# Optimization experiments

Measured on AMD Instinct MI355X. Metric: run time of the kernel, lower is better.

Reference implementation:

```python
import jax, jax.numpy as jnp
import numpy as np

N_NODES = 100000


def gcn_conv(x, src, dst, W, b, n):
    # PyG GCNConv: add self-loops, symmetric deg^-1/2 normalization,
    # linear transform, scatter-add aggregation, bias.
    loops = jnp.arange(n, dtype=src.dtype)
    s = jnp.concatenate([src, loops])
    d = jnp.concatenate([dst, loops])
    deg = jax.ops.segment_sum(jnp.ones_like(s, dtype=x.dtype), d, num_segments=n)
    dinv = jnp.where(deg > 0, jax.lax.rsqrt(deg), 0.0)
    norm = dinv[s] * dinv[d]  # [E+N]
    h = x @ W  # [N, out]
    msgs = h[s] * norm[:, None]  # gather + scale, [E+N, out]
    out = jax.ops.segment_sum(msgs, d, num_segments=n)  # scatter-add
    return out + b


def setup_inputs() -> dict:
    key = jax.random.key(0)
    k1, k2, k3, k4 = jax.random.split(key, 4)
    n, e = N_NODES, 1600000
    cin, chid, cout = 256, 128, 64
    x = jax.random.normal(k1, (n, cin), dtype=jnp.float32)
    edge_index = jax.random.randint(k2, (2, e), 0, n, dtype=jnp.int64)
    W1 = jax.random.normal(k3, (cin, chid), dtype=jnp.float32) * (1.0 / np.sqrt(cin))
    b1 = jnp.zeros((chid,), dtype=jnp.float32)
    W2 = jax.random.normal(k4, (chid, cout), dtype=jnp.float32) * (1.0 / np.sqrt(chid))
    b2 = jnp.zeros((cout,), dtype=jnp.float32)
    return {"x": x, "edge_index": edge_index, "W1": W1, "b1": b1, "W2": W2, "b2": b2}


def reference(x, edge_index, W1, b1, W2, b2):
    n = x.shape[0]
    src, dst = edge_index[0], edge_index[1]
    h = gcn_conv(x, src, dst, W1, b1, n)
    h = jax.nn.relu(h)
    # dropout is identity in eval mode (training=False)
    out = gcn_conv(h, src, dst, W2, b2, n)
    return out
```

## Files before the change

### kernel.cpp

```cpp
#include <hip/hip_runtime.h>


constexpr int NB_SHIFT = 7;
constexpr int NB_MAX   = 1024;
constexpr int BCAP     = 4096;
constexpr int BHIST    = 256;

__device__ __forceinline__ float bf2f(ushort u) {
    return __uint_as_float((unsigned)u << 16);
}
__device__ __forceinline__ ushort f2bf(float f) {
    unsigned u = __float_as_uint(f);
    return (ushort)((u + 0x7FFF + ((u >> 16) & 1)) >> 16);
}

__global__ __launch_bounds__(256) void k_hist(const int* __restrict__ dst,
                                              int* __restrict__ ghist,
                                              int E, int NB, int epb) {
    __shared__ int h[NB_MAX];
    const int t = threadIdx.x;
    for (int b = t; b < NB; b += 256) h[b] = 0;
    __syncthreads();
    const int e0 = blockIdx.x * epb;
    const int e1 = min(E, e0 + epb);
    for (int e = e0 + t; e < e1; e += 256) atomicAdd(&h[dst[e] >> NB_SHIFT], 1);
    __syncthreads();
    for (int b = t; b < NB; b += 256) ghist[b * gridDim.x + blockIdx.x] = h[b];
}

template <int TPB>
__global__ void k_scanL1(const int* __restrict__ in, int* __restrict__ out,
                         int* __restrict__ bsum, int ntot) {
    __shared__ int s[TPB];
    const int t = threadIdx.x;
    const int g = blockIdx.x * TPB + t;
    int v = (g < ntot) ? in[g] : 0;
    s[t] = v;
    __syncthreads();
    #pragma unroll
    for (int d = 1; d < TPB; d <<= 1) {
        int x = (t >= d) ? s[t - d] : 0;
        __syncthreads();
        s[t] += x;
        __syncthreads();
    }
    if (g < ntot) out[g] = s[t] - v;
    if (t == TPB - 1) bsum[blockIdx.x] = s[t];
}

__global__ void k_scanL2(int* __restrict__ bsum, int nb) {
    __shared__ int s[512];
    const int t = threadIdx.x;
    int v = (t < nb) ? bsum[t] : 0;
    s[t] = v;
    __syncthreads();
    #pragma unroll
    for (int d = 1; d < 512; d <<= 1) {
        int x = (t >= d) ? s[t - d] : 0;
        __syncthreads();
        s[t] += x;
        __syncthreads();
    }
    if (t < nb) bsum[t] = s[t] - v;
}

__global__ __launch_bounds__(256) void k_scatter(const int* __restrict__ src,
                                                 const int* __restrict__ dst,
                                                 const int* __restrict__ scan,
                                                 const int* __restrict__ bsum,
                                                 int2* __restrict__ pairs,
                                                 int E, int NB, int epb) {
    __shared__ int cur[NB_MAX];
    const int t = threadIdx.x;
    const int B = gridDim.x;
    const int blk = blockIdx.x;
    for (int b = t; b < NB; b += 256) {
        int idx = b * B + blk;
        cur[b] = scan[idx] + bsum[idx >> 9];
    }
    __syncthreads();
    const int e0 = blk * epb;
    const int e1 = min(E, e0 + epb);
    for (int e = e0 + t; e < e1; e += 256) {
        int d = dst[e];
        int slot = atomicAdd(&cur[d >> NB_SHIFT], 1);
        pairs[slot] = make_int2(src[e], d);
    }
}

__global__ __launch_bounds__(256) void k_build(const int2* __restrict__ pairs,
                                               const int* __restrict__ scan,
                                               const int* __restrict__ bsum,
                                               int* __restrict__ srcs,
                                               int* __restrict__ off,
                                               float* __restrict__ dinv,
                                               int n, int E, int NB, int B) {
    __shared__ int h[128], loff[128], curs[128];
    __shared__ int sb[BCAP];
    const int t = threadIdx.x;
    const int bk = blockIdx.x;
    const int i0 = bk * B;
    const int base = scan[i0] + bsum[i0 >> 9];
    const int nextbase = (bk + 1 < NB) ? (scan[i0 + B] + bsum[(i0 + B) >> 9]) : E;
    const int count = nextbase - base;
    if (t < 128) h[t] = 0;
    __syncthreads();
    for (int e = t; e < count; e += 256) atomicAdd(&h[pairs[base + e].y & 127], 1);
    __syncthreads();
    if (t < 128) loff[t] = h[t];
    __syncthreads();
    #pragma unroll
    for (int d = 1; d < 128; d <<= 1) {
        int x = 0;
        if (t < 128 && t >= d) x = loff[t - d];
        __syncthreads();
        if (t < 128) loff[t] += x;
        __syncthreads();
    }
    if (t < 128) curs[t] = loff[t] - h[t];
    __syncthreads();
    for (int e = t; e < count; e += 256) {
        int2 p = pairs[base + e];
        int slot = atomicAdd(&curs[p.y & 127], 1);
        if (slot < BCAP) sb[slot] = p.x;
        else srcs[base + slot] = p.x;
    }
    __syncthreads();
    const int lim = min(count, BCAP);
    for (int e = t; e < lim; e += 256) srcs[base + e] = sb[e];
    const int node0 = bk << NB_SHIFT;
    if (t < 128) {
        int node = node0 + t;
        if (node < n) {
            off[node] = base + (loff[t] - h[t]);
            dinv[node] = rsqrtf((float)(h[t] + 1));
        }
    }
    if (bk == 0 && t == 0) off[n] = E;
}

template <int K, int N, int BM, int BK, int TM, int TN>
__global__ __launch_bounds__(256) void k_gemm_bf16out(
    const float* __restrict__ A, const float* __restrict__ B,
    ushort* __restrict__ C, int M) {
    constexpr int BN = N;
    constexpr int NTX = BN / TN;
    __shared__ float As[BM][BK];
    __shared__ float Bs[BK][BN];
    const int t = threadIdx.x;
    const int tx = t % NTX;
    const int ty = t / NTX;
    const int row0 = blockIdx.x * BM;
    float acc[TM][TN] = {};
    for (int kc = 0; kc < K; kc += BK) {
        #pragma unroll
        for (int i = 0; i < BM * BK / (256 * 4); ++i) {
            int f = (t + i * 256) * 4;
            int r = f / BK, kq = f % BK;
            float4 v = make_float4(0.f, 0.f, 0.f, 0.f);
            if (row0 + r < M)
                v = *(const float4*)(A + (size_t)(row0 + r) * K + kc + kq);
            *(float4*)&As[r][kq] = v;
        }
        #pragma unroll
        for (int i = 0; i < BK * BN / (256 * 4); ++i) {
            int f = (t + i * 256) * 4;
            int r = f / BN, c = f % BN;
            *(float4*)&Bs[r][c] = *(const float4*)(B + (size_t)(kc + r) * N + c);
        }
        __syncthreads();
        #pragma unroll
        for (int kk = 0; kk < BK; ++kk) {
            float a[TM], b[TN];
            #pragma unroll
            for (int i = 0; i < TM; ++i) a[i] = As[ty * TM + i][kk];
            #pragma unroll
            for (int j = 0; j < TN; ++j) b[j] = Bs[kk][tx * TN + j];
            #pragma unroll
            for (int i = 0; i < TM; ++i)
                #pragma unroll
                for (int j = 0; j < TN; ++j)
                    acc[i][j] = fmaf(a[i], b[j], acc[i][j]);
        }
        __syncthreads();
    }
    #pragma unroll
    for (int i = 0; i < TM; ++i) {
        int r = row0 + ty * TM + i;
        if (r < M) {
            ushort4 o;
            o.x = f2bf(acc[i][0]);
            o.y = f2bf(acc[i][1]);
            o.z = f2bf(acc[i][2]);
            o.w = f2bf(acc[i][3]);
            *(ushort4*)(C + (size_t)r * N + tx * TN) = o;
        }
    }
}

__global__ __launch_bounds__(256) void k_agg_mm(
    const ushort* __restrict__ h, const int* __restrict__ off,
    const int* __restrict__ srcs, const float* __restrict__ dinv,
    const float* __restrict__ b1, const float* __restrict__ W2,
    ushort* __restrict__ h3, int n) {
    __shared__ ushort W2s[128 * 64];
    __shared__ float2 stage[256];
    const int tid = threadIdx.x;
    #pragma unroll
    for (int i = 0; i < 8; ++i) {
        int f = (tid + i * 256) * 4;
        float4 v = *(const float4*)&W2[f];
        ushort4 o;
        o.x = f2bf(v.x); o.y = f2bf(v.y); o.z = f2bf(v.z); o.w = f2bf(v.w);
        *(ushort4*)&W2s[f] = o;
    }
    __syncthreads();
    const int lane = tid & 63;
    const int wbase = tid & ~63;
    const int wid = blockIdx.x * 4 + (tid >> 6);
    if (wid >= n) return;
    const float di = dinv[wid];
    const int e0 = off[wid], e1 = off[wid + 1];
    const ushort2* hp = (const ushort2*)h + lane;
    ushort2 rs = hp[(size_t)wid * 64];
    float2 acc = make_float2(bf2f(rs.x) * di * di, bf2f(rs.y) * di * di);
    for (int e = e0; e < e1; e += 64) {
        int m = e1 - e;
        if (m > 64) m = 64;
        float2 pk = make_float2(0.f, 0.f);
        if (lane < m) {
            int s = srcs[e + lane];
            pk.x = __int_as_float(s);
            pk.y = dinv[s] * di;
        }
        stage[tid] = pk;
        const int R = (m + 7) & ~7;
        for (int j = 0; j < R; j += 8) {
            int a[8]; float w[8]; ushort2 v[8];
            #pragma unroll
            for (int k = 0; k < 8; ++k) {
                float2 sw = stage[wbase + j + k];
                a[k] = __float_as_int(sw.x);
                w[k] = sw.y;
            }
            #pragma unroll
            for (int k = 0; k < 8; ++k) v[k] = hp[(size_t)a[k] * 64];
            #pragma unroll
            for (int k = 0; k < 8; ++k) {
                acc.x = fmaf(bf2f(v[k].x), w[k], acc.x);
                acc.y = fmaf(bf2f(v[k].y), w[k], acc.y);
            }
        }
    }
    float2 bb = ((const float2*)b1)[lane];
    acc.x = fmaxf(acc.x + bb.x, 0.f);
    acc.y = fmaxf(acc.y + bb.y, 0.f);
    stage[tid] = acc;
    const float* row = (const float*)&stage[wbase];
    float s0 = 0.f, s1 = 0.f, s2 = 0.f, s3 = 0.f;
    #pragma unroll 8
    for (int k = 0; k < 128; k += 4) {
        s0 = fmaf(row[k + 0], bf2f(W2s[(k + 0) * 64 + lane]), s0);
        s1 = fmaf(row[k + 1], bf2f(W2s[(k + 1) * 64 + lane]), s1);
        s2 = fmaf(row[k + 2], bf2f(W2s[(k + 2) * 64 + lane]), s2);
        s3 = fmaf(row[k + 3], bf2f(W2s[(k + 3) * 64 + lane]), s3);
    }
    h3[(size_t)wid * 64 + lane] = f2bf((s0 + s1) + (s2 + s3));
}

__global__ __launch_bounds__(256) void k_aggregate64(
    const ushort* __restrict__ h, const int* __restrict__ off,
    const int* __restrict__ srcs, const float* __restrict__ dinv,
    const float* __restrict__ bias, float* __restrict__ out, int n) {
    __shared__ float2 stage[256];
    const int tid = threadIdx.x;
    const int lane = tid & 63;
    const int wbase = tid & ~63;
    int wid = (int)((blockIdx.x * (size_t)blockDim.x + tid) >> 6);
    if (wid >= n) return;
    const float di = dinv[wid];
    const int e0 = off[wid], e1 = off[wid + 1];
    const ushort* hl = h + lane;
    float acc = bf2f(hl[(size_t)wid * 64]) * di * di;
    for (int e = e0; e < e1; e += 64) {
        int m = e1 - e;
        if (m > 64) m = 64;
        float2 pk = make_float2(0.f, 0.f);
        if (lane < m) {
            int s = srcs[e + lane];
            pk.x = __int_as_float(s);
            pk.y = dinv[s] * di;
        }
        stage[tid] = pk;
        const int R = (m + 7) & ~7;
        for (int j = 0; j < R; j += 8) {
            int a[8]; float w[8]; ushort v[8];
            #pragma unroll
            for (int k = 0; k < 8; ++k) {
                float2 sw = stage[wbase + j + k];
                a[k] = __float_as_int(sw.x);
                w[k] = sw.y;
            }
            #pragma unroll
            for (int k = 0; k < 8; ++k) v[k] = hl[(size_t)a[k] * 64];
            #pragma unroll
            for (int k = 0; k < 8; ++k) acc = fmaf(bf2f(v[k]), w[k], acc);
        }
    }
    out[(size_t)wid * 64 + lane] = acc + bias[lane];
}

extern "C" void kernel_launch(void* const* d_in, const int* in_sizes, int n_in,
                              void* d_out, int out_size, void* d_ws, size_t ws_size,
                              hipStream_t stream) {
    const float* x  = (const float*)d_in[0];
    const int*   ei = (const int*)d_in[1];
    const float* W1 = (const float*)d_in[2];
    const float* b1 = (const float*)d_in[3];
    const float* W2 = (const float*)d_in[4];
    const float* b2 = (const float*)d_in[5];
    float* out = (float*)d_out;

    const int n = in_sizes[0] / 256;
    const int E = in_sizes[1] / 2;
    const int* src = ei;
    const int* dst = ei + E;

    const int NB  = (n + 127) >> NB_SHIFT;
    const int B   = BHIST;
    const int epb = (E + B - 1) / B;
    const int ntot = NB * B;
    const int gL1 = (ntot + 511) / 512;

    char* p = (char*)d_ws;
    auto alloc = [&](size_t bytes) {
        char* q = p;
        p += (bytes + 255) & ~(size_t)255;
        return q;
    };
    int*    ghist = (int*)alloc((size_t)ntot * 4);
    int*    scan  = (int*)alloc((size_t)ntot * 4);
    int*    bsum  = (int*)alloc(2048);
    int*    off   = (int*)alloc((size_t)(n + 1) * 4);
    float*  dinv  = (float*)alloc((size_t)n * 4);
    int*    srcs  = (int*)alloc((size_t)E * 4);
    ushort* h1    = (ushort*)alloc((size_t)n * 128 * 2);
    ushort* h3    = (ushort*)alloc((size_t)n * 64 * 2);
    int2*   pairs = (int2*)h1;

    k_hist<<<B, 256, 0, stream>>>(dst, ghist, E, NB, epb);
    k_scanL1<512><<<gL1, 512, 0, stream>>>(ghist, scan, bsum, ntot);
    k_scanL2<<<1, 512, 0, stream>>>(bsum, gL1);
    k_scatter<<<B, 256, 0, stream>>>(src, dst, scan, bsum, pairs, E, NB, epb);
    k_build<<<NB, 256, 0, stream>>>(pairs, scan, bsum, srcs, off, dinv, n, E, NB, B);

    k_gemm_bf16out<256, 128, 64, 32, 8, 4><<<(n + 63) / 64, 256, 0, stream>>>(x, W1, h1, n);
    k_agg_mm<<<(n + 3) / 4, 256, 0, stream>>>(h1, off, srcs, dinv, b1, W2, h3, n);
    k_aggregate64<<<(n + 3) / 4, 256, 0, stream>>>(h3, off, srcs, dinv, b2, out, n);
}
```

Before: 455.2 us.

## Use bf16 MFMA for first GEMM and precompute packed src/dinv edge array

Replaces the fp32 FMA tiled GEMM for x@W1 with a bf16 MFMA 16x16x32 kernel that converts A and W to bf16 in shared memory. It also adds a kernel that packs each edge's source index and dinv[src] into one float2 array. Both aggregation kernels then read this array instead of doing a dependent dinv gather per edge. The extra pass writes and reads 8 bytes per edge, and rounding the GEMM inputs to bf16 adds precision loss.

```diff
diff --git a/kernel.cpp b/kernel.cpp
--- a/kernel.cpp
+++ b/kernel.cpp
@@ -5,6 +5,9 @@
 constexpr int NB_MAX   = 1024;
 constexpr int BCAP     = 4096;
 constexpr int BHIST    = 256;
+
+typedef __attribute__((ext_vector_type(8))) short bf16x8;
+typedef __attribute__((ext_vector_type(4))) float f32x4;
 
 __device__ __forceinline__ float bf2f(ushort u) {
     return __uint_as_float((unsigned)u << 16);
@@ -139,68 +142,74 @@
     if (bk == 0 && t == 0) off[n] = E;
 }
 
-template <int K, int N, int BM, int BK, int TM, int TN>
-__global__ __launch_bounds__(256) void k_gemm_bf16out(
-    const float* __restrict__ A, const float* __restrict__ B,
+__global__ __launch_bounds__(256) void k_wfill(const int* __restrict__ srcs,
+                                               const float* __restrict__ dinv,
+                                               float2* __restrict__ sw, int E) {
+    int e = blockIdx.x * 256 + threadIdx.x;
+    if (e < E) {
+        int s = srcs[e];
+        sw[e] = make_float2(__int_as_float(s), dinv[s]);
+    }
+}
+
+__global__ __launch_bounds__(256) void k_gemm_mfma(
+    const float* __restrict__ A, const float* __restrict__ W,
     ushort* __restrict__ C, int M) {
-    constexpr int BN = N;
-    constexpr int NTX = BN / TN;
-    __shared__ float As[BM][BK];
-    __shared__ float Bs[BK][BN];
-    const int t = threadIdx.x;
-    const int tx = t % NTX;
-    const int ty = t / NTX;
-    const int row0 = blockIdx.x * BM;
-    float acc[TM][TN] = {};
-    for (int kc = 0; kc < K; kc += BK) {
+    __shared__ ushort As[64][32];
+    __shared__ ushort Bs[128][40];
+    const int t = threadIdx.x;
+    const int w = t >> 6;
+    const int l = t & 63;
+    const int row0 = blockIdx.x * 64;
+    f32x4 acc[8] = {};
+    for (int kc = 0; kc < 256; kc += 32) {
         #pragma unroll
-        for (int i = 0; i < BM * BK / (256 * 4); ++i) {
-            int f = (t + i * 256) * 4;
-            int r = f / BK, kq = f % BK;
-            float4 v = make_float4(0.f, 0.f, 0.f, 0.f);
-            if (row0 + r < M)
-                v = *(const float4*)(A + (size_t)(row0 + r) * K + kc + kq);
-            *(float4*)&As[r][kq] = v;
-        }
+        for (int i = 0; i < 8; ++i) {
+            int f = t + i * 256;
+            int r = f >> 5, c = f & 31;
+            float v = 0.f;
+            if (row0 + r < M) v = A[(size_t)(row0 + r) * 256 + kc + c];
+            As[r][c] = f2bf(v);
+        }
+        {
+            int c = t & 127;
+            int rr = t >> 7;
+            #pragma unroll
+            for (int i = 0; i < 8; ++i) {
+                int k0 = (rr * 8 + i) * 2;
+                ushort2 o;
+                o.x = f2bf(W[(size_t)(kc + k0) * 128 + c]);
+                o.y = f2bf(W[(size_t)(kc + k0 + 1) * 128 + c]);
+                *(ushort2*)&Bs[c][k0] = o;
+            }
+        }
+        __syncthreads();
+        const int kg = l >> 4;
+        const int lr = l & 15;
+        bf16x8 af = *(const bf16x8*)&As[w * 16 + lr][kg * 8];
         #pragma unroll
-        for (int i = 0; i < BK * BN / (256 * 4); ++i) {
-            int f = (t + i * 256) * 4;
-            int r = f / BN, c = f % BN;
-            *(float4*)&Bs[r][c] = *(const float4*)(B + (size_t)(kc + r) * N + c);
-        }
-        __syncthreads();
-        #pragma unroll
-        for (int kk = 0; kk < BK; ++kk) {
-            float a[TM], b[TN];
-            #pragma unroll
-            for (int i = 0; i < TM; ++i) a[i] = As[ty * TM + i][kk];
-            #pragma unroll
-            for (int j = 0; j < TN; ++j) b[j] = Bs[kk][tx * TN + j];
-            #pragma unroll
-            for (int i = 0; i < TM; ++i)
-                #pragma unroll
-                for (int j = 0; j < TN; ++j)
-                    acc[i][j] = fmaf(a[i], b[j], acc[i][j]);
-        }
-        __syncthreads();
-    }
-    #pragma unroll
-    for (int i = 0; i < TM; ++i) {
-        int r = row0 + ty * TM + i;
+        for (int nt = 0; nt < 8; ++nt) {
+            bf16x8 bf = *(const bf16x8*)&Bs[nt * 16 + lr][kg * 8];
+            acc[nt] = __builtin_amdgcn_mfma_f32_16x16x32_bf16(af, bf, acc[nt], 0, 0, 0);
+        }
+        __syncthreads();
+    }
+    const int mrow = (l >> 4) * 4;
+    const int col0 = l & 15;
+    #pragma unroll
+    for (int q = 0; q < 4; ++q) {
+        int r = row0 + w * 16 + mrow + q;
         if (r < M) {
-            ushort4 o;
-            o.x = f2bf(acc[i][0]);
-            o.y = f2bf(acc[i][1]);
-            o.z = f2bf(acc[i][2]);
-            o.w = f2bf(acc[i][3]);
-            *(ushort4*)(C + (size_t)r * N + tx * TN) = o;
+            #pragma unroll
+            for (int nt = 0; nt < 8; ++nt)
+                C[(size_t)r * 128 + nt * 16 + col0] = f2bf(acc[nt][q]);
         }
     }
 }
 
 __global__ __launch_bounds__(256) void k_agg_mm(
     const ushort* __restrict__ h, const int* __restrict__ off,
-    const int* __restrict__ srcs, const float* __restrict__ dinv,
+    const float2* __restrict__ sw, const float* __restrict__ dinv,
     const float* __restrict__ b1, const float* __restrict__ W2,
     ushort* __restrict__ h3, int n) {
     __shared__ ushort W2s[128 * 64];
@@ -229,9 +238,9 @@
         if (m > 64) m = 64;
         float2 pk = make_float2(0.f, 0.f);
         if (lane < m) {
-            int s = srcs[e + lane];
-            pk.x = __int_as_float(s);
-            pk.y = dinv[s] * di;
+            float2 s = sw[e + lane];
+            pk.x = s.x;
+            pk.y = s.y * di;
         }
         stage[tid] = pk;
         const int R = (m + 7) & ~7;
@@ -239,9 +248,9 @@
             int a[8]; float w[8]; ushort2 v[8];
             #pragma unroll
             for (int k = 0; k < 8; ++k) {
-                float2 sw = stage[wbase + j + k];
-                a[k] = __float_as_int(sw.x);
-                w[k] = sw.y;
+                float2 swv = stage[wbase + j + k];
+                a[k] = __float_as_int(swv.x);
+                w[k] = swv.y;
             }
             #pragma unroll
             for (int k = 0; k < 8; ++k) v[k] = hp[(size_t)a[k] * 64];
@@ -270,7 +279,7 @@
 
 __global__ __launch_bounds__(256) void k_aggregate64(
     const ushort* __restrict__ h, const int* __restrict__ off,
-    const int* __restrict__ srcs, const float* __restrict__ dinv,
+    const float2* __restrict__ sw, const float* __restrict__ dinv,
     const float* __restrict__ bias, float* __restrict__ out, int n) {
     __shared__ float2 stage[256];
     const int tid = threadIdx.x;
@@ -287,9 +296,9 @@
         if (m > 64) m = 64;
         float2 pk = make_float2(0.f, 0.f);
         if (lane < m) {
-            int s = srcs[e + lane];
-            pk.x = __int_as_float(s);
-            pk.y = dinv[s] * di;
+            float2 s = sw[e + lane];
+            pk.x = s.x;
+            pk.y = s.y * di;
         }
         stage[tid] = pk;
         const int R = (m + 7) & ~7;
@@ -297,9 +306,9 @@
             int a[8]; float w[8]; ushort v[8];
             #pragma unroll
             for (int k = 0; k < 8; ++k) {
-                float2 sw = stage[wbase + j + k];
-                a[k] = __float_as_int(sw.x);
-                w[k] = sw.y;
+                float2 swv = stage[wbase + j + k];
+                a[k] = __float_as_int(swv.x);
+                w[k] = swv.y;
             }
             #pragma unroll
             for (int k = 0; k < 8; ++k) v[k] = hl[(size_t)a[k] * 64];
@@ -344,6 +353,7 @@
     int*    off   = (int*)alloc((size_t)(n + 1) * 4);
     float*  dinv  = (float*)alloc((size_t)n * 4);
     int*    srcs  = (int*)alloc((size_t)E * 4);
+    float2* sw    = (float2*)alloc((size_t)E * 8);
     ushort* h1    = (ushort*)alloc((size_t)n * 128 * 2);
     ushort* h3    = (ushort*)alloc((size_t)n * 64 * 2);
     int2*   pairs = (int2*)h1;
@@ -353,8 +363,9 @@
     k_scanL2<<<1, 512, 0, stream>>>(bsum, gL1);
     k_scatter<<<B, 256, 0, stream>>>(src, dst, scan, bsum, pairs, E, NB, epb);
     k_build<<<NB, 256, 0, stream>>>(pairs, scan, bsum, srcs, off, dinv, n, E, NB, B);
-
-    k_gemm_bf16out<256, 128, 64, 32, 8, 4><<<(n + 63) / 64, 256, 0, stream>>>(x, W1, h1, n);
-    k_agg_mm<<<(n + 3) / 4, 256, 0, stream>>>(h1, off, srcs, dinv, b1, W2, h3, n);
-    k_aggregate64<<<(n + 3) / 4, 256, 0, stream>>>(h3, off, srcs, dinv, b2, out, n);
-}
+    k_wfill<<<(E + 255) / 256, 256, 0, stream>>>(srcs, dinv, sw, E);
+
+    k_gemm_mfma<<<(n + 63) / 64, 256, 0, stream>>>(x, W1, h1, n);
+    k_agg_mm<<<(n + 3) / 4, 256, 0, stream>>>(h1, off, sw, dinv, b1, W2, h3, n);
+    k_aggregate64<<<(n + 3) / 4, 256, 0, stream>>>(h3, off, sw, dinv, b2, out, n);
+}
```

After: 450.5 us. No clear change (-1.0%).
